# Kernel tuning notes

Hardware: AMD Instinct MI355X
Metric: run time of the kernel (lower is better)

Reference implementation:

```python
import jax, jax.numpy as jnp
import numpy as np

N_NODES = 50000


def _gcn_conv(x, W, b, src, dst, n):
    # GCNConv (PyG semantics): x' = D^-1/2 (A + I) D^-1/2 (x W) + b
    h = x @ W  # [N, out]
    loop = jnp.arange(n, dtype=src.dtype)
    s = jnp.concatenate([src, loop])  # self-loops appended
    d = jnp.concatenate([dst, loop])
    deg = jax.ops.segment_sum(jnp.ones_like(d, dtype=h.dtype), d, num_segments=n)
    dinv = jnp.where(deg > 0, jax.lax.rsqrt(deg), 0.0)
    norm = dinv[s] * dinv[d]  # [E+N]
    msgs = norm[:, None] * h[s]  # gather: [E+N, out]
    out = jax.ops.segment_sum(msgs, d, num_segments=n)  # scatter-add
    return out + b


def setup_inputs() -> dict:
    key = jax.random.key(0)
    ks = jax.random.split(key, 6)
    n, din, dh, dout, e = N_NODES, 64, 64, 16, 1600000
    x = jax.random.normal(ks[0], (n, din), dtype=jnp.float32)
    edge_index = jax.random.randint(ks[1], (2, e), 0, n, dtype=jnp.int64)
    W1 = jax.random.normal(ks[2], (din, dh), dtype=jnp.float32) / np.sqrt(din)
    b1 = jnp.zeros((dh,), dtype=jnp.float32)
    W2 = jax.random.normal(ks[3], (dh, dout), dtype=jnp.float32) / np.sqrt(dh)
    b2 = jnp.zeros((dout,), dtype=jnp.float32)
    return {"x": x, "edge_index": edge_index, "W1": W1, "b1": b1, "W2": W2, "b2": b2}


def reference(x, edge_index, W1, b1, W2, b2):
    n = x.shape[0]
    src, dst = edge_index[0], edge_index[1]
    h = _gcn_conv(x, W1, b1, src, dst, n)
    h = jax.nn.relu(h)
    h = _gcn_conv(h, W2, b2, src, dst, n)
    return jax.nn.log_softmax(h, axis=1)
```

## Files before the change

kernel.cpp:

```cpp
#include <hip/hip_runtime.h>
#include <hip/hip_bf16.h>
#include <math.h>

#define BSHIFT 6
#define BNODES 64
#define MAXB 1024
#define SORTCAP 4096
#define TILE 16

__device__ __forceinline__ bool detect_f64(const void* edges, long long nn) {
    const long long* e64 = (const long long*)edges;
    bool ok = true;
#pragma unroll
    for (int i = 0; i < 8; ++i) {
        long long v = e64[i];
        ok = ok && (v >= 0 && v < nn);
    }
    return ok;
}

__device__ __forceinline__ float bf16lo(unsigned int u) {
    return __uint_as_float(u << 16);
}
__device__ __forceinline__ float bf16hi(unsigned int u) {
    return __uint_as_float(u & 0xFFFF0000u);
}
__device__ __forceinline__ float bf16dec(unsigned short u) {
    return __uint_as_float(((unsigned int)u) << 16);
}
__device__ __forceinline__ unsigned short bf16enc(float f) {
    __hip_bfloat16 h = __float2bfloat16(f);
    return *reinterpret_cast<unsigned short*>(&h);
}

__global__ __launch_bounds__(512) void k_buckcount(const void* edges, long long nn,
                                                   long long E, int nbuckets, int* totals) {
    __shared__ int cnt[MAXB];
    int t = threadIdx.x;
    for (int b = t; b < nbuckets; b += 512) cnt[b] = 0;
    __syncthreads();
    bool f64 = detect_f64(edges, nn);
    long long chunk = (E + gridDim.x - 1) / gridDim.x;
    long long e0 = (long long)blockIdx.x * chunk;
    long long e1 = e0 + chunk; if (e1 > E) e1 = E;
    for (long long e = e0 + t; e < e1; e += 512) {
        int d = f64 ? (int)((const long long*)edges)[E + e] : ((const int*)edges)[E + e];
        atomicAdd(&cnt[d >> BSHIFT], 1);
    }
    __syncthreads();
    for (int b = t; b < nbuckets; b += 512)
        if (cnt[b] > 0) atomicAdd(&totals[b], cnt[b]);
}

__global__ __launch_bounds__(1024) void k_scan(const int* __restrict__ totals, int nbuckets,
                                               int* base, int* cursor) {
    __shared__ int tmp[MAXB];
    int t = threadIdx.x;
    int v = (t < nbuckets) ? totals[t] : 0;
    tmp[t] = v;
    __syncthreads();
    for (int off = 1; off < MAXB; off <<= 1) {
        int a = (t >= off) ? tmp[t - off] : 0;
        __syncthreads();
        tmp[t] += a;
        __syncthreads();
    }
    if (t < nbuckets) {
        int ex = tmp[t] - v;
        base[t] = ex;
        cursor[t] = ex;
    }
}

__global__ __launch_bounds__(512) void k_binscatter(const void* edges, long long nn,
                                                    long long E, int nbuckets, int* cursor,
                                                    unsigned int* keys) {
    __shared__ int cnt[MAXB];
    __shared__ int base_l[MAXB];
    int t = threadIdx.x;
    bool f64 = detect_f64(edges, nn);
    long long chunk = (E + gridDim.x - 1) / gridDim.x;
    long long e0 = (long long)blockIdx.x * chunk;
    long long e1 = e0 + chunk; if (e1 > E) e1 = E;
    for (long long tile0 = e0; tile0 < e1; tile0 += (long long)512 * TILE) {
        for (int b = t; b < nbuckets; b += 512) cnt[b] = 0;
        __syncthreads();
        int ss[TILE], dd[TILE];
#pragma unroll
        for (int j = 0; j < TILE; ++j) {
            long long e = tile0 + (long long)j * 512 + t;
            int s = 0, d = -1;
            if (e < e1) {
                if (f64) {
                    const long long* ee = (const long long*)edges;
                    s = (int)ee[e]; d = (int)ee[E + e];
                } else {
                    const int* ee = (const int*)edges;
                    s = ee[e]; d = ee[E + e];
                }
                atomicAdd(&cnt[d >> BSHIFT], 1);
            }
            ss[j] = s; dd[j] = d;
        }
        __syncthreads();
        for (int b = t; b < nbuckets; b += 512) {
            int c = cnt[b];
            base_l[b] = (c > 0) ? atomicAdd(&cursor[b], c) : 0;
            cnt[b] = 0;
        }
        __syncthreads();
#pragma unroll
        for (int j = 0; j < TILE; ++j) {
            int d = dd[j];
            if (d >= 0) {
                int b = d >> BSHIFT;
                int pos = base_l[b] + atomicAdd(&cnt[b], 1);
                keys[pos] = (unsigned int)ss[j] | ((unsigned int)(d & (BNODES - 1)) << 17);
            }
        }
        __syncthreads();
    }
}

__global__ __launch_bounds__(256) void k_sortdeg(unsigned int* keys,
                                                 const int* __restrict__ base,
                                                 const int* __restrict__ totals,
                                                 int* rowstart, int* counts,
                                                 float* dinv, int n,
                                                 unsigned int* scratch) {
    __shared__ unsigned int kbuf[SORTCAP];
    __shared__ int hist[BNODES];
    __shared__ int cur[BNODES];
    int t = threadIdx.x;
    int bk = blockIdx.x;
    int st = base[bk], c = totals[bk];
    if (t < BNODES) hist[t] = 0;
    __syncthreads();
    bool fits = (c <= SORTCAP);
    if (fits) {
        for (int i = t; i < c; i += 256) {
            unsigned int k = keys[st + i];
            kbuf[i] = k;
            atomicAdd(&hist[k >> 17], 1);
        }
    } else {
        for (int i = t; i < c; i += 256) {
            unsigned int k = keys[st + i];
            scratch[st + i] = k;
            atomicAdd(&hist[k >> 17], 1);
        }
    }
    __syncthreads();
    if (t < 64) {
        int v = hist[t];
        int incl = v;
        for (int o = 1; o < 64; o <<= 1) {
            int other = __shfl_up(incl, o, 64);
            if (t >= o) incl += other;
        }
        int ex = incl - v;
        cur[t] = ex;
        int node = bk * BNODES + t;
        if (node < n) {
            rowstart[node] = st + ex;
            counts[node] = v;
            dinv[node] = rsqrtf((float)v + 1.0f);
        }
    }
    __syncthreads();
    if (fits) {
        for (int i = t; i < c; i += 256) {
            unsigned int k = kbuf[i];
            int pos = atomicAdd(&cur[k >> 17], 1);
            keys[st + pos] = k & 0x1FFFFu;
        }
    } else {
        for (int i = t; i < c; i += 256) {
            unsigned int k = scratch[st + i];
            int pos = atomicAdd(&cur[k >> 17], 1);
            keys[st + pos] = k & 0x1FFFFu;
        }
    }
}

__global__ __launch_bounds__(256) void k_gemm1(const float* __restrict__ x,
                                               const float* __restrict__ W,
                                               const float* __restrict__ dinv,
                                               unsigned short* __restrict__ h) {
    __shared__ float Ws[64][64];
    __shared__ float xs[16][64];
    int t = threadIdx.x;
    for (int i = t; i < 64 * 64; i += 256) Ws[i >> 6][i & 63] = W[i];
    long long row0 = (long long)blockIdx.x * 16;
    ((float4*)xs)[t] = ((const float4*)(x + row0 * 64))[t];
    __syncthreads();
    int r = t >> 4, c0 = (t & 15) * 4;
    float4 acc = {0.f, 0.f, 0.f, 0.f};
#pragma unroll
    for (int k = 0; k < 64; ++k) {
        float xv = xs[r][k];
        float4 wv = *((const float4*)&Ws[k][c0]);
        acc.x += xv * wv.x; acc.y += xv * wv.y;
        acc.z += xv * wv.z; acc.w += xv * wv.w;
    }
    float di = dinv[row0 + r];
    ushort4 pk;
    pk.x = bf16enc(di * acc.x);
    pk.y = bf16enc(di * acc.y);
    pk.z = bf16enc(di * acc.z);
    pk.w = bf16enc(di * acc.w);
    *((ushort4*)(h + (row0 + r) * 64 + c0)) = pk;
}

__global__ __launch_bounds__(256) void k_gemm2(const unsigned short* __restrict__ h,
                                               const float* __restrict__ W,
                                               const float* __restrict__ dinv,
                                               unsigned short* __restrict__ h2) {
    __shared__ float Ws[64 * 16];
    __shared__ float xs[16][64];
    int t = threadIdx.x;
    for (int i = t; i < 64 * 16; i += 256) Ws[i] = W[i];
    long long row0 = (long long)blockIdx.x * 16;
    ushort4 u4 = ((const ushort4*)(h + row0 * 64))[t];
    int lr = t >> 4, lc = (t & 15) * 4;
    xs[lr][lc + 0] = bf16dec(u4.x);
    xs[lr][lc + 1] = bf16dec(u4.y);
    xs[lr][lc + 2] = bf16dec(u4.z);
    xs[lr][lc + 3] = bf16dec(u4.w);
    __syncthreads();
    int r = t >> 4, c = t & 15;
    float acc = 0.f;
#pragma unroll
    for (int k = 0; k < 64; ++k) acc += xs[r][k] * Ws[k * 16 + c];
    h2[(row0 + r) * 16 + c] = bf16enc(dinv[row0 + r] * acc);
}

__global__ __launch_bounds__(256) void k_agg64(const int* __restrict__ rowstart,
                                               const int* __restrict__ counts,
                                               const unsigned int* __restrict__ srcs,
                                               const unsigned int* __restrict__ hb2,
                                               const float* __restrict__ dinv,
                                               const float* __restrict__ b,
                                               unsigned short* __restrict__ out, int n) {
    int d = (blockIdx.x * 256 + threadIdx.x) >> 6;
    if (d >= n) return;
    int lane = threadIdx.x & 63;
    int half = lane >> 5;
    int fl = lane & 31;
    float ax = 0.f, ay = 0.f;
    if (half == 0) {
        unsigned int u = hb2[(long long)d * 32 + fl];
        ax = bf16lo(u); ay = bf16hi(u);
    }
    int start = rowstart[d];
    int cnt = counts[d];
    int k = 0;
    for (; k + 8 <= cnt; k += 8) {
        unsigned int s0 = srcs[start + k + half];
        unsigned int s1 = srcs[start + k + 2 + half];
        unsigned int s2 = srcs[start + k + 4 + half];
        unsigned int s3 = srcs[start + k + 6 + half];
        unsigned int u0 = hb2[(long long)s0 * 32 + fl];
        unsigned int u1 = hb2[(long long)s1 * 32 + fl];
        unsigned int u2 = hb2[(long long)s2 * 32 + fl];
        unsigned int u3 = hb2[(long long)s3 * 32 + fl];
        ax += bf16lo(u0); ay += bf16hi(u0);
        ax += bf16lo(u1); ay += bf16hi(u1);
        ax += bf16lo(u2); ay += bf16hi(u2);
        ax += bf16lo(u3); ay += bf16hi(u3);
    }
    for (; k < cnt; k += 2) {
        int idx = k + half;
        unsigned int u0 = 0;
        if (idx < cnt) u0 = hb2[(long long)srcs[start + idx] * 32 + fl];
        ax += bf16lo(u0); ay += bf16hi(u0);
    }
    ax += __shfl_xor(ax, 32);
    ay += __shfl_xor(ay, 32);
    float di = dinv[d];
    float2 bb = ((const float2*)b)[fl];
    float ox = fmaxf(di * ax + bb.x, 0.f);
    float oy = fmaxf(di * ay + bb.y, 0.f);
    if (half == 0) {
        unsigned int pk = (unsigned int)bf16enc(ox) | ((unsigned int)bf16enc(oy) << 16);
        ((unsigned int*)(out + (long long)d * 64))[fl] = pk;
    }
}

__global__ __launch_bounds__(256) void k_agg16(const int* __restrict__ rowstart,
                                               const int* __restrict__ counts,
                                               const unsigned int* __restrict__ srcs,
                                               const unsigned short* __restrict__ hb,
                                               const float* __restrict__ dinv,
                                               const float* __restrict__ b,
                                               float* __restrict__ out, int n) {
    int g = (blockIdx.x * 256 + threadIdx.x) >> 4;
    if (g >= n) return;
    int f = threadIdx.x & 15;
    long long rb = (long long)g * 16;
    float acc = bf16dec(hb[rb + f]);
    int start = rowstart[g];
    int cnt = counts[g];
    int k = 0;
    for (; k + 8 <= cnt; k += 8) {
        unsigned int s0 = srcs[start + k];
        unsigned int s1 = srcs[start + k + 1];
        unsigned int s2 = srcs[start + k + 2];
        unsigned int s3 = srcs[start + k + 3];
        unsigned int s4 = srcs[start + k + 4];
        unsigned int s5 = srcs[start + k + 5];
        unsigned int s6 = srcs[start + k + 6];
        unsigned int s7 = srcs[start + k + 7];
        unsigned short u0 = hb[(long long)s0 * 16 + f];
        unsigned short u1 = hb[(long long)s1 * 16 + f];
        unsigned short u2 = hb[(long long)s2 * 16 + f];
        unsigned short u3 = hb[(long long)s3 * 16 + f];
        unsigned short u4 = hb[(long long)s4 * 16 + f];
        unsigned short u5 = hb[(long long)s5 * 16 + f];
        unsigned short u6 = hb[(long long)s6 * 16 + f];
        unsigned short u7 = hb[(long long)s7 * 16 + f];
        acc += bf16dec(u0); acc += bf16dec(u1); acc += bf16dec(u2); acc += bf16dec(u3);
        acc += bf16dec(u4); acc += bf16dec(u5); acc += bf16dec(u6); acc += bf16dec(u7);
    }
    for (; k < cnt; ++k) acc += bf16dec(hb[(long long)srcs[start + k] * 16 + f]);
    float v = dinv[g] * acc + b[f];
    float m = v;
#pragma unroll
    for (int o = 8; o >= 1; o >>= 1) m = fmaxf(m, __shfl_xor(m, o, 16));
    float ex = __expf(v - m);
#pragma unroll
    for (int o = 8; o >= 1; o >>= 1) ex += __shfl_xor(ex, o, 16);
    out[rb + f] = (v - m) - __logf(ex);
}

extern "C" void kernel_launch(void* const* d_in, const int* in_sizes, int n_in,
                              void* d_out, int out_size, void* d_ws, size_t ws_size,
                              hipStream_t stream) {
    const float* x  = (const float*)d_in[0];
    const void*  ei = d_in[1];
    const float* W1 = (const float*)d_in[2];
    const float* b1 = (const float*)d_in[3];
    const float* W2 = (const float*)d_in[4];
    const float* b2 = (const float*)d_in[5];

    long long dh  = in_sizes[3];
    long long din = in_sizes[2] / dh;
    long long n   = in_sizes[0] / din;
    long long E   = (long long)in_sizes[1] / 2;
    int nbuckets  = (int)((n + BNODES - 1) >> BSHIFT);

    char* ws = (char*)d_ws;
    auto alloc = [&](size_t bytes) { void* p = ws; ws += (bytes + 255) & ~255ULL; return p; };
    int*   totals   = (int*)alloc(nbuckets * 4);
    int*   base     = (int*)alloc(nbuckets * 4);
    int*   cursor   = (int*)alloc(nbuckets * 4);
    int*   rowstart = (int*)alloc(n * 4);
    int*   counts   = (int*)alloc(n * 4);
    float* dinv     = (float*)alloc(n * 4);
    unsigned int* keys = (unsigned int*)alloc(E * 4);
    unsigned short* h1b  = (unsigned short*)alloc(n * 64 * 2);
    unsigned short* out1 = (unsigned short*)alloc(n * 64 * 2);
    unsigned short* h2b  = (unsigned short*)alloc(n * 16 * 2);
    unsigned int* sort_scratch = (unsigned int*)out1;

    float* out = (float*)d_out;

    hipMemsetAsync(totals, 0, (size_t)nbuckets * 4, stream);

    k_buckcount<<<256, 512, 0, stream>>>(ei, n, E, nbuckets, totals);
    k_scan<<<1, 1024, 0, stream>>>(totals, nbuckets, base, cursor);
    k_binscatter<<<256, 512, 0, stream>>>(ei, n, E, nbuckets, cursor, keys);
    k_sortdeg<<<nbuckets, 256, 0, stream>>>(keys, base, totals, rowstart, counts,
                                            dinv, (int)n, sort_scratch);

    k_gemm1<<<(int)(n / 16), 256, 0, stream>>>(x, W1, dinv, h1b);
    k_agg64<<<(int)((n * 64 + 255) / 256), 256, 0, stream>>>(
        rowstart, counts, keys, (const unsigned int*)h1b, dinv, b1, out1, (int)n);

    k_gemm2<<<(int)(n / 16), 256, 0, stream>>>(out1, W2, dinv, h2b);
    k_agg16<<<(int)((n * 16 + 255) / 256), 256, 0, stream>>>(
        rowstart, counts, keys, h2b, dinv, b2, out, (int)n);
}
```

Measured before the change: 134.3 us.

## Fuse bucket scan into count kernel and widen aggregation gather loads

Folds the single-block prefix scan into k_buckcount using a last-block-done atomic counter, which removes one kernel launch. The two aggregation kernels are reworked so each lane loads wider vectors: k_agg64 splits a wavefront into four edge groups reading uint2 (four bf16 values), and k_agg16 splits 16 lanes into two edge groups reading packed bf16 pairs, with shuffle reductions to combine them. The aim is fewer, wider memory transactions and more edges in flight per wavefront. In exchange it adds extra shuffle reductions and depends on correct threadfence and atomic ordering in the last-block scan.

```diff
diff --git a/kernel.cpp b/kernel.cpp
--- a/kernel.cpp
+++ b/kernel.cpp
@@ -34,8 +34,11 @@
 }
 
 __global__ __launch_bounds__(512) void k_buckcount(const void* edges, long long nn,
-                                                   long long E, int nbuckets, int* totals) {
+                                                   long long E, int nbuckets, int* totals,
+                                                   int* base, int* cursor) {
     __shared__ int cnt[MAXB];
+    __shared__ int tmp[512];
+    __shared__ int lastflag;
     int t = threadIdx.x;
     for (int b = t; b < nbuckets; b += 512) cnt[b] = 0;
     __syncthreads();
@@ -50,26 +53,27 @@
     __syncthreads();
     for (int b = t; b < nbuckets; b += 512)
         if (cnt[b] > 0) atomicAdd(&totals[b], cnt[b]);
-}
-
-__global__ __launch_bounds__(1024) void k_scan(const int* __restrict__ totals, int nbuckets,
-                                               int* base, int* cursor) {
-    __shared__ int tmp[MAXB];
-    int t = threadIdx.x;
-    int v = (t < nbuckets) ? totals[t] : 0;
-    tmp[t] = v;
-    __syncthreads();
-    for (int off = 1; off < MAXB; off <<= 1) {
+    __threadfence();
+    if (t == 0) {
+        int r = atomicAdd(&totals[nbuckets], 1);
+        lastflag = (r == (int)gridDim.x - 1);
+    }
+    __syncthreads();
+    if (!lastflag) return;
+    int i0 = 2 * t, i1 = 2 * t + 1;
+    int a0 = (i0 < nbuckets) ? atomicAdd(&totals[i0], 0) : 0;
+    int a1 = (i1 < nbuckets) ? atomicAdd(&totals[i1], 0) : 0;
+    tmp[t] = a0 + a1;
+    __syncthreads();
+    for (int off = 1; off < 512; off <<= 1) {
         int a = (t >= off) ? tmp[t - off] : 0;
         __syncthreads();
         tmp[t] += a;
         __syncthreads();
     }
-    if (t < nbuckets) {
-        int ex = tmp[t] - v;
-        base[t] = ex;
-        cursor[t] = ex;
-    }
+    int ex = tmp[t] - (a0 + a1);
+    if (i0 < nbuckets) { base[i0] = ex; cursor[i0] = ex; }
+    if (i1 < nbuckets) { base[i1] = ex + a0; cursor[i1] = ex + a0; }
 }
 
 __global__ __launch_bounds__(512) void k_binscatter(const void* edges, long long nn,
@@ -238,99 +242,122 @@
 __global__ __launch_bounds__(256) void k_agg64(const int* __restrict__ rowstart,
                                                const int* __restrict__ counts,
                                                const unsigned int* __restrict__ srcs,
-                                               const unsigned int* __restrict__ hb2,
+                                               const uint2* __restrict__ hb4,
                                                const float* __restrict__ dinv,
                                                const float* __restrict__ b,
                                                unsigned short* __restrict__ out, int n) {
     int d = (blockIdx.x * 256 + threadIdx.x) >> 6;
     if (d >= n) return;
     int lane = threadIdx.x & 63;
-    int half = lane >> 5;
-    int fl = lane & 31;
-    float ax = 0.f, ay = 0.f;
-    if (half == 0) {
-        unsigned int u = hb2[(long long)d * 32 + fl];
-        ax = bf16lo(u); ay = bf16hi(u);
+    int q = lane >> 4;
+    int fl = lane & 15;
+    float a0 = 0.f, a1 = 0.f, a2 = 0.f, a3 = 0.f;
+    if (q == 0) {
+        uint2 u = hb4[(long long)d * 16 + fl];
+        a0 = bf16lo(u.x); a1 = bf16hi(u.x); a2 = bf16lo(u.y); a3 = bf16hi(u.y);
     }
     int start = rowstart[d];
     int cnt = counts[d];
     int k = 0;
-    for (; k + 8 <= cnt; k += 8) {
-        unsigned int s0 = srcs[start + k + half];
-        unsigned int s1 = srcs[start + k + 2 + half];
-        unsigned int s2 = srcs[start + k + 4 + half];
-        unsigned int s3 = srcs[start + k + 6 + half];
-        unsigned int u0 = hb2[(long long)s0 * 32 + fl];
-        unsigned int u1 = hb2[(long long)s1 * 32 + fl];
-        unsigned int u2 = hb2[(long long)s2 * 32 + fl];
-        unsigned int u3 = hb2[(long long)s3 * 32 + fl];
-        ax += bf16lo(u0); ay += bf16hi(u0);
-        ax += bf16lo(u1); ay += bf16hi(u1);
-        ax += bf16lo(u2); ay += bf16hi(u2);
-        ax += bf16lo(u3); ay += bf16hi(u3);
-    }
-    for (; k < cnt; k += 2) {
-        int idx = k + half;
-        unsigned int u0 = 0;
-        if (idx < cnt) u0 = hb2[(long long)srcs[start + idx] * 32 + fl];
-        ax += bf16lo(u0); ay += bf16hi(u0);
-    }
-    ax += __shfl_xor(ax, 32);
-    ay += __shfl_xor(ay, 32);
-    float di = dinv[d];
-    float2 bb = ((const float2*)b)[fl];
-    float ox = fmaxf(di * ax + bb.x, 0.f);
-    float oy = fmaxf(di * ay + bb.y, 0.f);
-    if (half == 0) {
-        unsigned int pk = (unsigned int)bf16enc(ox) | ((unsigned int)bf16enc(oy) << 16);
-        ((unsigned int*)(out + (long long)d * 64))[fl] = pk;
+    for (; k + 16 <= cnt; k += 16) {
+        unsigned int s0 = srcs[start + k + q];
+        unsigned int s1 = srcs[start + k + 4 + q];
+        unsigned int s2 = srcs[start + k + 8 + q];
+        unsigned int s3 = srcs[start + k + 12 + q];
+        uint2 u0 = hb4[(long long)s0 * 16 + fl];
+        uint2 u1 = hb4[(long long)s1 * 16 + fl];
+        uint2 u2 = hb4[(long long)s2 * 16 + fl];
+        uint2 u3 = hb4[(long long)s3 * 16 + fl];
+        a0 += bf16lo(u0.x); a1 += bf16hi(u0.x); a2 += bf16lo(u0.y); a3 += bf16hi(u0.y);
+        a0 += bf16lo(u1.x); a1 += bf16hi(u1.x); a2 += bf16lo(u1.y); a3 += bf16hi(u1.y);
+        a0 += bf16lo(u2.x); a1 += bf16hi(u2.x); a2 += bf16lo(u2.y); a3 += bf16hi(u2.y);
+        a0 += bf16lo(u3.x); a1 += bf16hi(u3.x); a2 += bf16lo(u3.y); a3 += bf16hi(u3.y);
+    }
+    for (; k < cnt; k += 4) {
+        int idx = k + q;
+        if (idx < cnt) {
+            uint2 u = hb4[(long long)srcs[start + idx] * 16 + fl];
+            a0 += bf16lo(u.x); a1 += bf16hi(u.x); a2 += bf16lo(u.y); a3 += bf16hi(u.y);
+        }
+    }
+    a0 += __shfl_xor(a0, 16); a0 += __shfl_xor(a0, 32);
+    a1 += __shfl_xor(a1, 16); a1 += __shfl_xor(a1, 32);
+    a2 += __shfl_xor(a2, 16); a2 += __shfl_xor(a2, 32);
+    a3 += __shfl_xor(a3, 16); a3 += __shfl_xor(a3, 32);
+    if (q == 0) {
+        float di = dinv[d];
+        float4 bb = ((const float4*)b)[fl];
+        float o0 = fmaxf(di * a0 + bb.x, 0.f);
+        float o1 = fmaxf(di * a1 + bb.y, 0.f);
+        float o2 = fmaxf(di * a2 + bb.z, 0.f);
+        float o3 = fmaxf(di * a3 + bb.w, 0.f);
+        uint2 pk;
+        pk.x = (unsigned int)bf16enc(o0) | ((unsigned int)bf16enc(o1) << 16);
+        pk.y = (unsigned int)bf16enc(o2) | ((unsigned int)bf16enc(o3) << 16);
+        ((uint2*)(out + (long long)d * 64))[fl] = pk;
     }
 }
 
 __global__ __launch_bounds__(256) void k_agg16(const int* __restrict__ rowstart,
                                                const int* __restrict__ counts,
                                                const unsigned int* __restrict__ srcs,
-                                               const unsigned short* __restrict__ hb,
+                                               const unsigned int* __restrict__ hb2,
                                                const float* __restrict__ dinv,
                                                const float* __restrict__ b,
                                                float* __restrict__ out, int n) {
     int g = (blockIdx.x * 256 + threadIdx.x) >> 4;
     if (g >= n) return;
-    int f = threadIdx.x & 15;
-    long long rb = (long long)g * 16;
-    float acc = bf16dec(hb[rb + f]);
+    int lane = threadIdx.x & 15;
+    int h = lane >> 3;
+    int f8 = lane & 7;
+    float ax = 0.f, ay = 0.f;
+    if (h == 0) {
+        unsigned int u = hb2[(long long)g * 8 + f8];
+        ax = bf16lo(u); ay = bf16hi(u);
+    }
     int start = rowstart[g];
     int cnt = counts[g];
     int k = 0;
     for (; k + 8 <= cnt; k += 8) {
-        unsigned int s0 = srcs[start + k];
-        unsigned int s1 = srcs[start + k + 1];
-        unsigned int s2 = srcs[start + k + 2];
-        unsigned int s3 = srcs[start + k + 3];
-        unsigned int s4 = srcs[start + k + 4];
-        unsigned int s5 = srcs[start + k + 5];
-        unsigned int s6 = srcs[start + k + 6];
-        unsigned int s7 = srcs[start + k + 7];
-        unsigned short u0 = hb[(long long)s0 * 16 + f];
-        unsigned short u1 = hb[(long long)s1 * 16 + f];
-        unsigned short u2 = hb[(long long)s2 * 16 + f];
-        unsigned short u3 = hb[(long long)s3 * 16 + f];
-        unsigned short u4 = hb[(long long)s4 * 16 + f];
-        unsigned short u5 = hb[(long long)s5 * 16 + f];
-        unsigned short u6 = hb[(long long)s6 * 16 + f];
-        unsigned short u7 = hb[(long long)s7 * 16 + f];
-        acc += bf16dec(u0); acc += bf16dec(u1); acc += bf16dec(u2); acc += bf16dec(u3);
-        acc += bf16dec(u4); acc += bf16dec(u5); acc += bf16dec(u6); acc += bf16dec(u7);
-    }
-    for (; k < cnt; ++k) acc += bf16dec(hb[(long long)srcs[start + k] * 16 + f]);
-    float v = dinv[g] * acc + b[f];
-    float m = v;
-#pragma unroll
-    for (int o = 8; o >= 1; o >>= 1) m = fmaxf(m, __shfl_xor(m, o, 16));
-    float ex = __expf(v - m);
-#pragma unroll
-    for (int o = 8; o >= 1; o >>= 1) ex += __shfl_xor(ex, o, 16);
-    out[rb + f] = (v - m) - __logf(ex);
+        unsigned int s0 = srcs[start + k + h];
+        unsigned int s1 = srcs[start + k + 2 + h];
+        unsigned int s2 = srcs[start + k + 4 + h];
+        unsigned int s3 = srcs[start + k + 6 + h];
+        unsigned int u0 = hb2[(long long)s0 * 8 + f8];
+        unsigned int u1 = hb2[(long long)s1 * 8 + f8];
+        unsigned int u2 = hb2[(long long)s2 * 8 + f8];
+        unsigned int u3 = hb2[(long long)s3 * 8 + f8];
+        ax += bf16lo(u0); ay += bf16hi(u0);
+        ax += bf16lo(u1); ay += bf16hi(u1);
+        ax += bf16lo(u2); ay += bf16hi(u2);
+        ax += bf16lo(u3); ay += bf16hi(u3);
+    }
+    for (; k < cnt; k += 2) {
+        int idx = k + h;
+        if (idx < cnt) {
+            unsigned int u = hb2[(long long)srcs[start + idx] * 8 + f8];
+            ax += bf16lo(u); ay += bf16hi(u);
+        }
+    }
+    ax += __shfl_xor(ax, 8);
+    ay += __shfl_xor(ay, 8);
+    float di = dinv[g];
+    float2 bb = ((const float2*)b)[f8];
+    float v0 = di * ax + bb.x;
+    float v1 = di * ay + bb.y;
+    float m = fmaxf(v0, v1);
+#pragma unroll
+    for (int o = 4; o >= 1; o >>= 1) m = fmaxf(m, __shfl_xor(m, o));
+    float ex = __expf(v0 - m) + __expf(v1 - m);
+#pragma unroll
+    for (int o = 4; o >= 1; o >>= 1) ex += __shfl_xor(ex, o);
+    float lse = __logf(ex);
+    if (h == 0) {
+        float2 o2;
+        o2.x = (v0 - m) - lse;
+        o2.y = (v1 - m) - lse;
+        ((float2*)(out + (long long)g * 16))[f8] = o2;
+    }
 }
 
 extern "C" void kernel_launch(void* const* d_in, const int* in_sizes, int n_in,
@@ -351,7 +378,7 @@
 
     char* ws = (char*)d_ws;
     auto alloc = [&](size_t bytes) { void* p = ws; ws += (bytes + 255) & ~255ULL; return p; };
-    int*   totals   = (int*)alloc(nbuckets * 4);
+    int*   totals   = (int*)alloc((nbuckets + 1) * 4);
     int*   base     = (int*)alloc(nbuckets * 4);
     int*   cursor   = (int*)alloc(nbuckets * 4);
     int*   rowstart = (int*)alloc(n * 4);
@@ -365,19 +392,18 @@
 
     float* out = (float*)d_out;
 
-    hipMemsetAsync(totals, 0, (size_t)nbuckets * 4, stream);
-
-    k_buckcount<<<256, 512, 0, stream>>>(ei, n, E, nbuckets, totals);
-    k_scan<<<1, 1024, 0, stream>>>(totals, nbuckets, base, cursor);
+    hipMemsetAsync(totals, 0, (size_t)(nbuckets + 1) * 4, stream);
+
+    k_buckcount<<<256, 512, 0, stream>>>(ei, n, E, nbuckets, totals, base, cursor);
     k_binscatter<<<256, 512, 0, stream>>>(ei, n, E, nbuckets, cursor, keys);
     k_sortdeg<<<nbuckets, 256, 0, stream>>>(keys, base, totals, rowstart, counts,
                                             dinv, (int)n, sort_scratch);
 
     k_gemm1<<<(int)(n / 16), 256, 0, stream>>>(x, W1, dinv, h1b);
     k_agg64<<<(int)((n * 64 + 255) / 256), 256, 0, stream>>>(
-        rowstart, counts, keys, (const unsigned int*)h1b, dinv, b1, out1, (int)n);
+        rowstart, counts, keys, (const uint2*)h1b, dinv, b1, out1, (int)n);
 
     k_gemm2<<<(int)(n / 16), 256, 0, stream>>>(out1, W2, dinv, h2b);
     k_agg16<<<(int)((n * 16 + 255) / 256), 256, 0, stream>>>(
-        rowstart, counts, keys, h2b, dinv, b2, out, (int)n);
-}
+        rowstart, counts, keys, (const unsigned int*)h2b, dinv, b2, out, (int)n);
+}
```

New measurement: 152.0 us. 13.2% more time.

## Replace atomic bucket binning with per-block histogram and two-level scan placement

Applied to the files above, without the earlier changes.

Bucketing edges by destination now uses per-block histograms written to a partial array, a per-bucket scan over blocks plus a global scan to get each block's exact offsets, and a placement kernel that only uses shared-memory atomic cursors. This removes the global atomics on bucket cursors, the tiled register staging in the scatter kernel, and the memset. The cost is an extra kernel launch and a partial-count array of buckets times blocks. Key order within a bucket is no longer fixed, but the later sort stage handles that.

```diff
diff --git a/kernel.cpp b/kernel.cpp
--- a/kernel.cpp
+++ b/kernel.cpp
@@ -6,7 +6,6 @@
 #define BNODES 64
 #define MAXB 1024
 #define SORTCAP 4096
-#define TILE 16
 
 __device__ __forceinline__ bool detect_f64(const void* edges, long long nn) {
     const long long* e64 = (const long long*)edges;
@@ -33,27 +32,43 @@
     return *reinterpret_cast<unsigned short*>(&h);
 }
 
-__global__ __launch_bounds__(512) void k_buckcount(const void* edges, long long nn,
-                                                   long long E, int nbuckets, int* totals) {
+__global__ __launch_bounds__(512) void k_hist(const void* edges, long long nn,
+                                              long long E, long long epb,
+                                              int nbuckets, int nblk, int* partial) {
     __shared__ int cnt[MAXB];
     int t = threadIdx.x;
+    int i = blockIdx.x;
     for (int b = t; b < nbuckets; b += 512) cnt[b] = 0;
     __syncthreads();
     bool f64 = detect_f64(edges, nn);
-    long long chunk = (E + gridDim.x - 1) / gridDim.x;
-    long long e0 = (long long)blockIdx.x * chunk;
-    long long e1 = e0 + chunk; if (e1 > E) e1 = E;
+    long long e0 = (long long)i * epb;
+    long long e1 = e0 + epb; if (e1 > E) e1 = E;
     for (long long e = e0 + t; e < e1; e += 512) {
         int d = f64 ? (int)((const long long*)edges)[E + e] : ((const int*)edges)[E + e];
         atomicAdd(&cnt[d >> BSHIFT], 1);
     }
     __syncthreads();
-    for (int b = t; b < nbuckets; b += 512)
-        if (cnt[b] > 0) atomicAdd(&totals[b], cnt[b]);
+    for (int b = t; b < nbuckets; b += 512) partial[b * nblk + i] = cnt[b];
+}
+
+__global__ __launch_bounds__(256) void k_scanB(int* partial, int nblk, int* totals) {
+    __shared__ int tmp[256];
+    int b = blockIdx.x, t = threadIdx.x;
+    int v = (t < nblk) ? partial[b * nblk + t] : 0;
+    tmp[t] = v;
+    __syncthreads();
+    for (int off = 1; off < 256; off <<= 1) {
+        int a = (t >= off) ? tmp[t - off] : 0;
+        __syncthreads();
+        tmp[t] += a;
+        __syncthreads();
+    }
+    if (t < nblk) partial[b * nblk + t] = tmp[t] - v;
+    if (t == 255) totals[b] = tmp[255];
 }
 
 __global__ __launch_bounds__(1024) void k_scan(const int* __restrict__ totals, int nbuckets,
-                                               int* base, int* cursor) {
+                                               int* base) {
     __shared__ int tmp[MAXB];
     int t = threadIdx.x;
     int v = (t < nbuckets) ? totals[t] : 0;
@@ -65,60 +80,34 @@
         tmp[t] += a;
         __syncthreads();
     }
-    if (t < nbuckets) {
-        int ex = tmp[t] - v;
-        base[t] = ex;
-        cursor[t] = ex;
-    }
-}
-
-__global__ __launch_bounds__(512) void k_binscatter(const void* edges, long long nn,
-                                                    long long E, int nbuckets, int* cursor,
-                                                    unsigned int* keys) {
-    __shared__ int cnt[MAXB];
-    __shared__ int base_l[MAXB];
-    int t = threadIdx.x;
+    if (t < nbuckets) base[t] = tmp[t] - v;
+}
+
+__global__ __launch_bounds__(512) void k_place(const void* edges, long long nn,
+                                               long long E, long long epb,
+                                               int nbuckets, int nblk,
+                                               const int* __restrict__ base,
+                                               const int* __restrict__ partial,
+                                               unsigned int* keys) {
+    __shared__ int cur[MAXB];
+    int t = threadIdx.x;
+    int i = blockIdx.x;
+    for (int b = t; b < nbuckets; b += 512) cur[b] = base[b] + partial[b * nblk + i];
+    __syncthreads();
     bool f64 = detect_f64(edges, nn);
-    long long chunk = (E + gridDim.x - 1) / gridDim.x;
-    long long e0 = (long long)blockIdx.x * chunk;
-    long long e1 = e0 + chunk; if (e1 > E) e1 = E;
-    for (long long tile0 = e0; tile0 < e1; tile0 += (long long)512 * TILE) {
-        for (int b = t; b < nbuckets; b += 512) cnt[b] = 0;
-        __syncthreads();
-        int ss[TILE], dd[TILE];
-#pragma unroll
-        for (int j = 0; j < TILE; ++j) {
-            long long e = tile0 + (long long)j * 512 + t;
-            int s = 0, d = -1;
-            if (e < e1) {
-                if (f64) {
-                    const long long* ee = (const long long*)edges;
-                    s = (int)ee[e]; d = (int)ee[E + e];
-                } else {
-                    const int* ee = (const int*)edges;
-                    s = ee[e]; d = ee[E + e];
-                }
-                atomicAdd(&cnt[d >> BSHIFT], 1);
-            }
-            ss[j] = s; dd[j] = d;
-        }
-        __syncthreads();
-        for (int b = t; b < nbuckets; b += 512) {
-            int c = cnt[b];
-            base_l[b] = (c > 0) ? atomicAdd(&cursor[b], c) : 0;
-            cnt[b] = 0;
-        }
-        __syncthreads();
-#pragma unroll
-        for (int j = 0; j < TILE; ++j) {
-            int d = dd[j];
-            if (d >= 0) {
-                int b = d >> BSHIFT;
-                int pos = base_l[b] + atomicAdd(&cnt[b], 1);
-                keys[pos] = (unsigned int)ss[j] | ((unsigned int)(d & (BNODES - 1)) << 17);
-            }
-        }
-        __syncthreads();
+    long long e0 = (long long)i * epb;
+    long long e1 = e0 + epb; if (e1 > E) e1 = E;
+    for (long long e = e0 + t; e < e1; e += 512) {
+        int s, d;
+        if (f64) {
+            const long long* ee = (const long long*)edges;
+            s = (int)ee[e]; d = (int)ee[E + e];
+        } else {
+            const int* ee = (const int*)edges;
+            s = ee[e]; d = ee[E + e];
+        }
+        int pos = atomicAdd(&cur[d >> BSHIFT], 1);
+        keys[pos] = (unsigned int)s | ((unsigned int)(d & (BNODES - 1)) << 17);
     }
 }
 
@@ -349,14 +338,18 @@
     long long E   = (long long)in_sizes[1] / 2;
     int nbuckets  = (int)((n + BNODES - 1) >> BSHIFT);
 
+    long long epb = 8192;
+    while ((E + epb - 1) / epb > 256) epb <<= 1;
+    int nblk = (int)((E + epb - 1) / epb);
+
     char* ws = (char*)d_ws;
     auto alloc = [&](size_t bytes) { void* p = ws; ws += (bytes + 255) & ~255ULL; return p; };
     int*   totals   = (int*)alloc(nbuckets * 4);
     int*   base     = (int*)alloc(nbuckets * 4);
-    int*   cursor   = (int*)alloc(nbuckets * 4);
     int*   rowstart = (int*)alloc(n * 4);
     int*   counts   = (int*)alloc(n * 4);
     float* dinv     = (float*)alloc(n * 4);
+    int*   partial  = (int*)alloc((size_t)nbuckets * nblk * 4);
     unsigned int* keys = (unsigned int*)alloc(E * 4);
     unsigned short* h1b  = (unsigned short*)alloc(n * 64 * 2);
     unsigned short* out1 = (unsigned short*)alloc(n * 64 * 2);
@@ -365,11 +358,10 @@
 
     float* out = (float*)d_out;
 
-    hipMemsetAsync(totals, 0, (size_t)nbuckets * 4, stream);
-
-    k_buckcount<<<256, 512, 0, stream>>>(ei, n, E, nbuckets, totals);
-    k_scan<<<1, 1024, 0, stream>>>(totals, nbuckets, base, cursor);
-    k_binscatter<<<256, 512, 0, stream>>>(ei, n, E, nbuckets, cursor, keys);
+    k_hist<<<nblk, 512, 0, stream>>>(ei, n, E, epb, nbuckets, nblk, partial);
+    k_scanB<<<nbuckets, 256, 0, stream>>>(partial, nblk, totals);
+    k_scan<<<1, 1024, 0, stream>>>(totals, nbuckets, base);
+    k_place<<<nblk, 512, 0, stream>>>(ei, n, E, epb, nbuckets, nblk, base, partial, keys);
     k_sortdeg<<<nbuckets, 256, 0, stream>>>(keys, base, totals, rowstart, counts,
                                             dinv, (int)n, sort_scratch);
 
```

New measurement: 123.7 us. 7.8% less time.
